# Optimization experiments

Hardware: AMD Instinct MI355X
Metric: run time of the kernel (lower is better)

Reference implementation:

```python
import jax, jax.numpy as jnp
import numpy as np

N = 1024      # params.input_dim (f1 is a square [N, N] similarity matrix)
TOPK = 16     # params.topk
B = 64        # hardcoded batch in the original reshape
W = 2 * N // B  # spatial width after reshape


def setup_inputs() -> dict:
    key = jax.random.key(0)
    k1, k2, k3 = jax.random.split(key, 3)
    f1 = jax.random.normal(k1, (N, N), dtype=jnp.float32)
    # Conv2d(in=N, out=N, kernel=(TOPK, 1)) weights, kaiming-ish scale
    conv_w = jax.random.normal(k2, (N, N, TOPK, 1), dtype=jnp.float32) * 0.01
    conv_b = jax.random.normal(k3, (N,), dtype=jnp.float32) * 0.01
    return {"f1": f1, "conv_w": conv_w, "conv_b": conv_b}


def reference(f1, conv_w, conv_b):
    # i = topk indices along last dim (largest, sorted) -> [N, TOPK]
    _, idx = jax.lax.top_k(f1, TOPK)
    # pos = f1[i]: gather rows of f1 by the topk column indices -> [N, TOPK, N]
    pos = f1[idx]
    # repeat_interleave(TOPK, dim=0).reshape(N, TOPK, -1) == each row tiled TOPK times
    rep = jnp.broadcast_to(f1[:, None, :], (N, TOPK, N))
    # cat on dim=2 -> [N, TOPK, 2N]; reshape to NCHW [B, N, TOPK, W]
    out = jnp.concatenate([rep, pos], axis=2).reshape(B, N, TOPK, W)
    # Conv2d kernel (TOPK, 1), VALID padding collapses H -> 1: [B, N, 1, W]
    y = jax.lax.conv_general_dilated(
        out, conv_w, window_strides=(1, 1), padding='VALID',
        dimension_numbers=('NCHW', 'OIHW', 'NCHW'))
    y = y + conv_b[None, :, None, None]
    return jax.nn.relu(y).reshape(N, -1)  # [N, B*W] = [N, 2N]
```

## Files before the change

kernel.cpp:

```cpp
#include <hip/hip_runtime.h>
#include <stdint.h>


#define NDIM 1024
#define TK   16
#define KPOS 8192
#define KREP 512
#define NCOL 2048

typedef unsigned short u16;
typedef uint32_t u32;
typedef u16   u16x8  __attribute__((ext_vector_type(8)));
typedef __bf16 bf16x8 __attribute__((ext_vector_type(8)));
typedef float  f32x4  __attribute__((ext_vector_type(4)));

__device__ __forceinline__ u16 f2bf(float x) {
    union { float f; unsigned u; } v; v.f = x;
    unsigned r = 0x7FFFu + ((v.u >> 16) & 1u);
    return (u16)((v.u + r) >> 16);
}

__device__ __forceinline__ void load_lds_16B(const u16* g, u16* l) {
    __builtin_amdgcn_global_load_lds(
        (__attribute__((address_space(1))) void*)(uintptr_t)g,
        (__attribute__((address_space(3))) void*)(unsigned)(uintptr_t)l,
        16, 0, 0);
}

#define PREP_TOPK 256
#define PREP_ZERO 512
#define PREP_W    1024
#define PREP_F1T  256

__global__ __launch_bounds__(256) void prep_kernel(const float* __restrict__ f1,
                                                   const float* __restrict__ W,
                                                   int* __restrict__ idx,
                                                   u16* __restrict__ Wb,
                                                   u16* __restrict__ W1b,
                                                   u16* __restrict__ f1t,
                                                   float* __restrict__ out) {
    const int bid = blockIdx.x;
    const int t = threadIdx.x;
    if (bid < PREP_TOPK) {
        const int lane = t & 63;
        const int row  = bid * 4 + (t >> 6);
        float v[16];
        const float* src = f1 + row * NDIM + lane;
        #pragma unroll
        for (int j = 0; j < 16; ++j) v[j] = src[j * 64];
        for (int sel = 0; sel < TK; ++sel) {
            float best = -3.402823466e38f; int bg = 0x7fffffff;
            #pragma unroll
            for (int j = 0; j < 16; ++j)
                if (v[j] > best) { best = v[j]; bg = j * 64 + lane; }
            #pragma unroll
            for (int s = 1; s < 64; s <<= 1) {
                float ov = __shfl_xor(best, s);
                int   og = __shfl_xor(bg, s);
                if (ov > best || (ov == best && og < bg)) { best = ov; bg = og; }
            }
            if (lane == sel) idx[row * TK + sel] = bg;
            #pragma unroll
            for (int j = 0; j < 16; ++j)
                if (bg == j * 64 + lane) v[j] = -3.402823466e38f;
        }
    } else if (bid < PREP_TOPK + PREP_ZERO) {
        const int zb = bid - PREP_TOPK;
        f32x4 z = {0.f, 0.f, 0.f, 0.f};
        float* p = out + (size_t)zb * 4096 + t * 16;
        #pragma unroll
        for (int j = 0; j < 4; ++j) *(f32x4*)(p + j * 4) = z;
    } else if (bid < PREP_TOPK + PREP_ZERO + PREP_W) {
        const int o = bid - PREP_TOPK - PREP_ZERO;
        const float* wrow = W + (size_t)o * 16384;
        u16* wbrow = Wb + (size_t)o * KPOS;
        #pragma unroll
        for (int j = 0; j < 4; ++j) {
            const int v = j * 2048 + t * 8;
            const int u = ((v >> 5) << 6) + 32 + (v & 31);
            float4 a = *(const float4*)(wrow + u);
            float4 b = *(const float4*)(wrow + u + 4);
            u16x8 ov;
            ov[0] = f2bf(a.x); ov[1] = f2bf(a.y); ov[2] = f2bf(a.z); ov[3] = f2bf(a.w);
            ov[4] = f2bf(b.x); ov[5] = f2bf(b.y); ov[6] = f2bf(b.z); ov[7] = f2bf(b.w);
            *(u16x8*)(wbrow + v) = ov;
        }
        #pragma unroll
        for (int h = 0; h < 2; ++h) {
            const int kr = h * 256 + t;
            const int nl = kr >> 5, e = kr & 31;
            const float* base = wrow + nl * 1024 + e;
            float s = 0.f;
            #pragma unroll
            for (int tt = 0; tt < 16; ++tt) s += base[tt * 64];
            W1b[o * KREP + kr] = f2bf(s);
        }
    } else {
        const int gb = bid - PREP_TOPK - PREP_ZERO - PREP_W;
        const int unit = t >> 5;
        const int w = t & 31;
        const int rq = gb * 8 + unit;
        const int row = rq >> 1, q = rq & 1;
        const float* src = f1 + row * NDIM + q * 512;
        const int swp = ((w >> 2) & 1) * 8;
        u16 tmp[16];
        #pragma unroll
        for (int kh = 0; kh < 16; ++kh)
            tmp[kh ^ swp] = f2bf(src[kh * 32 + w]);
        u16* dst = f1t + ((size_t)row * 2 + q) * 512 + w * 16;
        *(u16x8*)(dst)     = *(u16x8*)(tmp);
        *(u16x8*)(dst + 8) = *(u16x8*)(tmp + 8);
    }
}

#define BM 128
#define BN 128
#define BK 64
#define KITERS 34

__global__ __launch_bounds__(256, 2) void gemm_kernel(const u16* __restrict__ Ap,
                                                      const u16* __restrict__ A1,
                                                      const u16* __restrict__ f1t,
                                                      const int* __restrict__ idx,
                                                      float* __restrict__ out) {
    __shared__ __align__(16) u16 As[2][BM * BK];
    __shared__ __align__(16) u16 Bs[2][16 * 512];
    __shared__ int idxL[256];
    const int f = blockIdx.x;
    const int m = f >> 6;
    const int u = f & 63;
    const int n = u & 15;
    const int z = u >> 4;
    const int t    = threadIdx.x;
    const int lane = t & 63;
    const int wave = t >> 6;
    const int wm   = (wave >> 1) * 64;
    const int wn   = (wave & 1) * 64;
    const int quad = lane >> 4;
    const int l16  = lane & 15;
    const int sw   = l16 & 7;
    const int o0 = m * BM;
    const int n0 = n * BN;
    const int nb0 = n * 4;
    const int kb = z * 2048;
    const int nl0 = z * 4;

    {
        const int bl = t >> 6, nlz = (t >> 4) & 3, tt = t & 15;
        idxL[t] = idx[((nb0 + bl) * 16 + nl0 + nlz) * TK + tt];
    }

    f32x4 acc[4][4] = {};

    const int rA = t >> 3;
    const int c8 = t & 7;
    const int csw = (c8 ^ (rA & 7)) * 8;
    const u16* gApos = Ap + (size_t)(o0 + rA) * KPOS + kb + csw;
    const u16* gArep = A1 + (size_t)(o0 + rA) * KREP + z * 128 + csw;
    const int ipbp = kb >> 4;
    const int ipbr = z * 8;

    auto stage = [&](int it, int nb) {
        u16* lA = As[nb] + t * 8;
        int rows[4], qp;
        if (it < 32) {
            const int k0 = it * BK;
            #pragma unroll
            for (int c = 0; c < 4; ++c)
                load_lds_16B(gApos + (size_t)(c * 32) * KPOS + k0, lA + c * 2048);
            const int ip = ipbp + it * 4 + wave;
            qp = ip & 1;
            const int nlz = (ip >> 5) & 3, tt = (ip >> 1) & 15;
            #pragma unroll
            for (int bl = 0; bl < 4; ++bl)
                rows[bl] = idxL[bl * 64 + nlz * 16 + tt];
        } else {
            const int k0 = (it - 32) * BK;
            #pragma unroll
            for (int c = 0; c < 4; ++c)
                load_lds_16B(gArep + (size_t)(c * 32) * KREP + k0, lA + c * 2048);
            const int ip = ipbr + (it - 32) * 4 + wave;
            qp = ip & 1;
            const int nlr = ip >> 1;
            #pragma unroll
            for (int bl = 0; bl < 4; ++bl)
                rows[bl] = (nb0 + bl) * 16 + nlr;
        }
        #pragma unroll
        for (int bl = 0; bl < 4; ++bl)
            load_lds_16B(f1t + ((size_t)rows[bl] * 2 + qp) * 512 + lane * 8,
                         Bs[nb] + (wave * 4 + bl) * 512);
    };

    __syncthreads();
    stage(0, 0);
    __syncthreads();

    for (int it = 0; it < KITERS; ++it) {
        const int cur = it & 1;
        if (it + 1 < KITERS) stage(it + 1, 1 - cur);

        #pragma unroll
        for (int ks = 0; ks < 2; ++ks) {
            bf16x8 af[4], bfr[4];
            #pragma unroll
            for (int mt = 0; mt < 4; ++mt) {
                u16x8 bits = *(const u16x8*)(As[cur] + (wm + mt * 16 + l16) * BK
                                                + (((ks * 4 + quad) ^ sw) * 8));
                af[mt] = __builtin_bit_cast(bf16x8, bits);
            }
            const int ci2 = ks * 2 + (quad >> 1);
            const int qh  = quad & 1;
            #pragma unroll
            for (int nt = 0; nt < 4; ++nt) {
                const int nn = wn + nt * 16 + l16;
                const int blocf = nn >> 5, w = nn & 31;
                u16x8 bits = *(const u16x8*)(Bs[cur] + (ci2 * 4 + blocf) * 512 + w * 16
                                                + ((qh ^ ((w >> 2) & 1)) * 8));
                bfr[nt] = __builtin_bit_cast(bf16x8, bits);
            }
            #pragma unroll
            for (int mt = 0; mt < 4; ++mt)
                #pragma unroll
                for (int nt = 0; nt < 4; ++nt)
                    acc[mt][nt] = __builtin_amdgcn_mfma_f32_16x16x32_bf16(
                        af[mt], bfr[nt], acc[mt][nt], 0, 0, 0);
        }
        __syncthreads();
    }

    #pragma unroll
    for (int nt = 0; nt < 4; ++nt) {
        const int nn = n0 + wn + nt * 16 + l16;
        const int bb = nn >> 5, w = nn & 31;
        #pragma unroll
        for (int mt = 0; mt < 4; ++mt) {
            #pragma unroll
            for (int r = 0; r < 4; ++r) {
                const int o = o0 + wm + mt * 16 + quad * 4 + r;
                unsafeAtomicAdd(out + (size_t)(bb * 16 + (o >> 6)) * 2048
                                    + (o & 63) * 32 + w,
                                acc[mt][nt][r]);
            }
        }
    }
}

__global__ __launch_bounds__(256) void finalize_kernel(float* __restrict__ out,
                                                       const float* __restrict__ bias) {
    const int tid = blockIdx.x * 256 + threadIdx.x;
    const int f = tid * 4;
    const int o = ((f >> 11) & 15) * 64 + ((f & 2047) >> 5);
    const float bv = bias[o];
    float4 x = *(float4*)(out + f);
    x.x = fmaxf(x.x + bv, 0.f);
    x.y = fmaxf(x.y + bv, 0.f);
    x.z = fmaxf(x.z + bv, 0.f);
    x.w = fmaxf(x.w + bv, 0.f);
    *(float4*)(out + f) = x;
}

extern "C" void kernel_launch(void* const* d_in, const int* in_sizes, int n_in,
                              void* d_out, int out_size, void* d_ws, size_t ws_size,
                              hipStream_t stream) {
    const float* f1   = (const float*)d_in[0];
    const float* Wc   = (const float*)d_in[1];
    const float* bias = (const float*)d_in[2];
    float* out = (float*)d_out;

    int* idx = (int*)d_ws;
    u16* Wb  = (u16*)((char*)d_ws + 65536);
    u16* W1b = (u16*)((char*)d_ws + 16842752);
    u16* f1t = (u16*)((char*)d_ws + 17891328);

    prep_kernel<<<PREP_TOPK + PREP_ZERO + PREP_W + PREP_F1T,
                  256, 0, stream>>>(f1, Wc, idx, Wb, W1b, f1t, out);
    gemm_kernel<<<512, 256, 0, stream>>>(Wb, W1b, f1t, idx, out);
    finalize_kernel<<<(NDIM * NCOL) / (4 * 256), 256, 0, stream>>>(out, bias);
}
```

Before: 164.5 us.

## Load gathered B operand directly from global, double split-K, raise occupancy

The GEMM stops staging the gathered f1t rows into LDS and has each lane read its B fragments straight from global memory, using a precomputed per-block table of row offsets. The split-K factor doubles (1024 blocks, 17 K-iterations each) and the m index is moved to the low bits of the block id so neighbouring blocks share B rows in cache. Dropping the B LDS buffers allows a launch bound of 4 blocks per SIMD group. The trade-off is that B operand loads now sit on the critical path with global-memory latency instead of being prefetched, and twice as many atomic or partial-sum writes go to the output.

New measurement: 184.0 us. 1.12x slower.

```diff
diff --git a/kernel.cpp b/kernel.cpp
--- a/kernel.cpp
+++ b/kernel.cpp
@@ -116,21 +116,20 @@
 #define BM 128
 #define BN 128
 #define BK 64
-#define KITERS 34
-
-__global__ __launch_bounds__(256, 2) void gemm_kernel(const u16* __restrict__ Ap,
+#define KITERS 17
+
+__global__ __launch_bounds__(256, 4) void gemm_kernel(const u16* __restrict__ Ap,
                                                       const u16* __restrict__ A1,
                                                       const u16* __restrict__ f1t,
                                                       const int* __restrict__ idx,
                                                       float* __restrict__ out) {
     __shared__ __align__(16) u16 As[2][BM * BK];
-    __shared__ __align__(16) u16 Bs[2][16 * 512];
-    __shared__ int idxL[256];
+    __shared__ __align__(8) int idxO[272];
     const int f = blockIdx.x;
-    const int m = f >> 6;
-    const int u = f & 63;
-    const int n = u & 15;
-    const int z = u >> 4;
+    const int m = f & 7;
+    const int g = f >> 3;
+    const int n = g & 15;
+    const int z = g >> 4;
     const int t    = threadIdx.x;
     const int lane = t & 63;
     const int wave = t >> 6;
@@ -142,12 +141,20 @@
     const int o0 = m * BM;
     const int n0 = n * BN;
     const int nb0 = n * 4;
-    const int kb = z * 2048;
-    const int nl0 = z * 4;
+    const int kb = z * 1024;
 
     {
-        const int bl = t >> 6, nlz = (t >> 4) & 3, tt = t & 15;
-        idxL[t] = idx[((nb0 + bl) * 16 + nl0 + nlz) * TK + tt];
+        const int j = t >> 2, bl = t & 3;
+        const int ip = z * 64 + j;
+        const int nl = ip >> 5, tt = (ip >> 1) & 15, q = ip & 1;
+        const int row = idx[((nb0 + bl) * 16 + nl) * TK + tt];
+        idxO[j * 4 + bl] = ((row << 1) + q) << 9;
+        if (t < 16) {
+            const int ci = t >> 2, bl2 = t & 3;
+            const int ur = z * 4 + ci;
+            const int rrow = (nb0 + bl2) * 16 + (ur >> 1);
+            idxO[(64 + ci) * 4 + bl2] = ((rrow << 1) + (ur & 1)) << 9;
+        }
     }
 
     f32x4 acc[4][4] = {};
@@ -156,43 +163,29 @@
     const int c8 = t & 7;
     const int csw = (c8 ^ (rA & 7)) * 8;
     const u16* gApos = Ap + (size_t)(o0 + rA) * KPOS + kb + csw;
-    const u16* gArep = A1 + (size_t)(o0 + rA) * KREP + z * 128 + csw;
-    const int ipbp = kb >> 4;
-    const int ipbr = z * 8;
+    const u16* gArep = A1 + (size_t)(o0 + rA) * KREP + z * 64 + csw;
 
     auto stage = [&](int it, int nb) {
         u16* lA = As[nb] + t * 8;
-        int rows[4], qp;
-        if (it < 32) {
+        if (it < 16) {
             const int k0 = it * BK;
             #pragma unroll
             for (int c = 0; c < 4; ++c)
                 load_lds_16B(gApos + (size_t)(c * 32) * KPOS + k0, lA + c * 2048);
-            const int ip = ipbp + it * 4 + wave;
-            qp = ip & 1;
-            const int nlz = (ip >> 5) & 3, tt = (ip >> 1) & 15;
-            #pragma unroll
-            for (int bl = 0; bl < 4; ++bl)
-                rows[bl] = idxL[bl * 64 + nlz * 16 + tt];
         } else {
-            const int k0 = (it - 32) * BK;
             #pragma unroll
             for (int c = 0; c < 4; ++c)
-                load_lds_16B(gArep + (size_t)(c * 32) * KREP + k0, lA + c * 2048);
-            const int ip = ipbr + (it - 32) * 4 + wave;
-            qp = ip & 1;
-            const int nlr = ip >> 1;
-            #pragma unroll
-            for (int bl = 0; bl < 4; ++bl)
-                rows[bl] = (nb0 + bl) * 16 + nlr;
-        }
-        #pragma unroll
-        for (int bl = 0; bl < 4; ++bl)
-            load_lds_16B(f1t + ((size_t)rows[bl] * 2 + qp) * 512 + lane * 8,
-                         Bs[nb] + (wave * 4 + bl) * 512);
+                load_lds_16B(gArep + (size_t)(c * 32) * KREP, lA + c * 2048);
+        }
     };
 
-    __syncthreads();
+    const int qh = quad & 1;
+    const int sel = (qh ^ ((l16 >> 2) & 1)) * 8;
+    const u16* Bb0 = f1t + l16 * 16 + sel;
+    const u16* Bb1 = f1t + (16 + l16) * 16 + sel;
+    const int ci2base = quad >> 1;
+    const int blh = (wave & 1) * 2;
+
     stage(0, 0);
     __syncthreads();
 
@@ -200,8 +193,10 @@
         const int cur = it & 1;
         if (it + 1 < KITERS) stage(it + 1, 1 - cur);
 
+        const int jb = (it < 16) ? it * 4 : 64;
         #pragma unroll
         for (int ks = 0; ks < 2; ++ks) {
+            const int2 offp = *(const int2*)(&idxO[(jb + ks * 2 + ci2base) * 4 + blh]);
             bf16x8 af[4], bfr[4];
             #pragma unroll
             for (int mt = 0; mt < 4; ++mt) {
@@ -209,15 +204,11 @@
                                                 + (((ks * 4 + quad) ^ sw) * 8));
                 af[mt] = __builtin_bit_cast(bf16x8, bits);
             }
-            const int ci2 = ks * 2 + (quad >> 1);
-            const int qh  = quad & 1;
             #pragma unroll
             for (int nt = 0; nt < 4; ++nt) {
-                const int nn = wn + nt * 16 + l16;
-                const int blocf = nn >> 5, w = nn & 31;
-                u16x8 bits = *(const u16x8*)(Bs[cur] + (ci2 * 4 + blocf) * 512 + w * 16
-                                                + ((qh ^ ((w >> 2) & 1)) * 8));
-                bfr[nt] = __builtin_bit_cast(bf16x8, bits);
+                const int off = (nt & 2) ? offp.y : offp.x;
+                const u16* p = ((nt & 1) ? Bb1 : Bb0) + off;
+                bfr[nt] = __builtin_bit_cast(bf16x8, *(const u16x8*)p);
             }
             #pragma unroll
             for (int mt = 0; mt < 4; ++mt)
@@ -275,6 +266,6 @@
 
     prep_kernel<<<PREP_TOPK + PREP_ZERO + PREP_W + PREP_F1T,
                   256, 0, stream>>>(f1, Wc, idx, Wb, W1b, f1t, out);
-    gemm_kernel<<<512, 256, 0, stream>>>(Wb, W1b, f1t, idx, out);
+    gemm_kernel<<<1024, 256, 0, stream>>>(Wb, W1b, f1t, idx, out);
     finalize_kernel<<<(NDIM * NCOL) / (4 * 256), 256, 0, stream>>>(out, bias);
 }
```
